# Kernel optimization log

Hardware: AMD Instinct MI355X
Metric: run time of the kernel (lower is better)

The kernel has to match this reference:

```python
import jax, jax.numpy as jnp
import numpy as np


def setup_inputs() -> dict:
    key = jax.random.key(0)
    ks = jax.random.split(key, 8)
    B, C, N = 4, 64, 32768
    d = C // 8
    inp = {
        "x": jax.random.normal(ks[0], (B, C, N), dtype=jnp.float32),
        "Wq": jax.random.normal(ks[1], (d, C), dtype=jnp.float32) * 0.1,
        "bq": jax.random.normal(ks[2], (d,), dtype=jnp.float32) * 0.1,
        "Wk": jax.random.normal(ks[3], (d, C), dtype=jnp.float32) * 0.1,
        "bk": jax.random.normal(ks[4], (d,), dtype=jnp.float32) * 0.1,
        "Wv": jax.random.normal(ks[5], (C, C), dtype=jnp.float32) * 0.1,
        "bv": jax.random.normal(ks[6], (C,), dtype=jnp.float32) * 0.1,
        # nn.Parameter(torch.zeros(1)) in the original; nonzero here so the
        # attention branch actually contributes to the output.
        "gamma": jax.random.normal(ks[7], (1,), dtype=jnp.float32) * 0.1,
        "window_size": 512,
        "stride": 256,
        "pooling_factor": 2,
    }
    return inp


def reference(x, Wq, bq, Wk, bk, Wv, bv, gamma, window_size, stride, pooling_factor):
    B, C, N = x.shape
    # conv1x1 projections are pointwise -> apply once on the full signal
    q = jnp.einsum("dc,bcn->bdn", Wq, x) + bq[None, :, None]  # [B, d, N]
    k = jnp.einsum("dc,bcn->bdn", Wk, x) + bk[None, :, None]  # [B, d, N]
    v = jnp.einsum("ec,bcn->ben", Wv, x) + bv[None, :, None]  # [B, C, N]

    starts = jnp.arange(0, N - window_size + 1, stride)              # [W]
    idx = starts[:, None] + jnp.arange(window_size)[None, :]         # [W, ws]

    qw = q[:, :, idx]  # [B, d, W, ws]
    kw = k[:, :, idx]
    vw = v[:, :, idx]  # [B, C, W, ws]
    xw = x[:, :, idx]

    energy = jnp.einsum("bdwi,bdwj->bwij", qw, kw)                   # [B, W, ws, ws]
    attn = jax.nn.softmax(energy, axis=-1)
    # torch: bmm(v, attn^T) -> out[c,i] = sum_j v[c,j] * attn[i,j]
    out_local = jnp.einsum("bcwj,bwij->bcwi", vw, attn)              # [B, C, W, ws]

    contrib = gamma[0] * out_local + xw
    out = jnp.zeros_like(x).at[:, :, idx].add(contrib)               # overlap-add
    counts = jnp.zeros((N,), x.dtype).at[idx].add(1.0)               # overlap count
    out = out / counts[None, None, :]

    P = pooling_factor
    Np = (N // P) * P
    out = out[:, :, :Np].reshape(B, C, N // P, P).max(axis=-1)       # MaxPool1d(P)
    return out
```

## Files before the change

### kernel.cpp

```cpp
#include <hip/hip_runtime.h>
#include <hip/hip_bf16.h>

#define BB 4
#define CC 64
#define DD 8
#define NN 32768
#define WW 512
#define STR 256
#define NWIN 127
#define LOG2E 1.4426950408889634f

typedef short bf16x8 __attribute__((ext_vector_type(8)));
typedef float f32x4 __attribute__((ext_vector_type(4)));

__device__ __forceinline__ unsigned int pack_bf16(float lo, float hi) {
    __hip_bfloat162 h = __float22bfloat162_rn(make_float2(lo, hi));
    unsigned int r; __builtin_memcpy(&r, &h, 4);
    return r;
}
__device__ __forceinline__ unsigned short to_bf16(float f) {
    __hip_bfloat16 h = __float2bfloat16(f);
    unsigned short r; __builtin_memcpy(&r, &h, 2);
    return r;
}
__device__ __forceinline__ float bf2f(unsigned short s) {
    union { unsigned int u; float f; } v; v.u = ((unsigned int)s) << 16;
    return v.f;
}
__device__ __forceinline__ float fast_exp2(float x) {
#if __has_builtin(__builtin_amdgcn_exp2f)
    return __builtin_amdgcn_exp2f(x);
#else
    float r; asm("v_exp_f32 %0, %1" : "=v"(r) : "v"(x)); return r;
#endif
}
__device__ __forceinline__ bf16x8 pack8(float a0, float a1, float a2, float a3,
                                        float a4, float a5, float a6, float a7) {
    union { bf16x8 v; unsigned int u[4]; } r;
    r.u[0] = pack_bf16(a0, a1); r.u[1] = pack_bf16(a2, a3);
    r.u[2] = pack_bf16(a4, a5); r.u[3] = pack_bf16(a6, a7);
    return r.v;
}

__global__ __launch_bounds__(256) void qkv_kernel(
    const float* __restrict__ x,
    const float* __restrict__ Wq, const float* __restrict__ bq,
    const float* __restrict__ Wk, const float* __restrict__ bk,
    const float* __restrict__ Wv, const float* __restrict__ bv,
    unsigned short* __restrict__ qout, unsigned short* __restrict__ kout,
    unsigned short* __restrict__ vout)
{
    const int t = threadIdx.x;
    const int lane = t & 63, wv = t >> 6;
    const int a = lane & 15, g = lane >> 4;

    bf16x8 wf[5][2];
    #pragma unroll
    for (int T = 0; T < 5; ++T) {
        const float* wrow;
        float scale = 1.f;
        if (T == 0) {
            if (a < 8) { wrow = Wq + a*CC; scale = LOG2E; }
            else       { wrow = Wk + (a-8)*CC; }
        } else {
            wrow = Wv + ((T-1)*16 + a)*CC;
        }
        #pragma unroll
        for (int h = 0; h < 2; ++h) {
            float4 w0 = *(const float4*)(wrow + h*32 + g*8);
            float4 w1 = *(const float4*)(wrow + h*32 + g*8 + 4);
            wf[T][h] = pack8(w0.x*scale, w0.y*scale, w0.z*scale, w0.w*scale,
                             w1.x*scale, w1.y*scale, w1.z*scale, w1.w*scale);
        }
    }
    f32x4 bias[5];
    {
        const int r = g*4;
        #pragma unroll
        for (int u = 0; u < 4; ++u) {
            int rr = r + u;
            bias[0][u] = (rr < 8) ? bq[rr]*LOG2E : bk[rr-8];
        }
        #pragma unroll
        for (int T = 1; T < 5; ++T)
            #pragma unroll
            for (int u = 0; u < 4; ++u)
                bias[T][u] = bv[(T-1)*16 + r + u];
    }

    const int wave_id = blockIdx.x*4 + wv;
    #pragma unroll 1
    for (int it = 0; it < 2; ++it) {
        const int chunk = wave_id + it*4096;
        const int b = chunk >> 11;
        const int n0 = (chunk & 2047) * 16;
        const int n = n0 + a;
        const float* xcol = x + (size_t)b*CC*NN + n;

        float xv0[8], xv1[8];
        #pragma unroll
        for (int u = 0; u < 8; ++u) xv0[u] = xcol[(size_t)(g*8 + u)*NN];
        #pragma unroll
        for (int u = 0; u < 8; ++u) xv1[u] = xcol[(size_t)(32 + g*8 + u)*NN];
        bf16x8 xb0 = pack8(xv0[0],xv0[1],xv0[2],xv0[3],xv0[4],xv0[5],xv0[6],xv0[7]);
        bf16x8 xb1 = pack8(xv1[0],xv1[1],xv1[2],xv1[3],xv1[4],xv1[5],xv1[6],xv1[7]);

        f32x4 acc[5];
        #pragma unroll
        for (int T = 0; T < 5; ++T) {
            acc[T] = __builtin_amdgcn_mfma_f32_16x16x32_bf16(wf[T][0], xb0, bias[T], 0, 0, 0);
            acc[T] = __builtin_amdgcn_mfma_f32_16x16x32_bf16(wf[T][1], xb1, acc[T], 0, 0, 0);
        }

        {
            unsigned int lo = pack_bf16(acc[0][0], acc[0][1]);
            unsigned int hi = pack_bf16(acc[0][2], acc[0][3]);
            unsigned short* base = ((g < 2) ? qout : kout) + ((size_t)b*NN + n)*8 + (g & 1)*4;
            *(int2*)base = make_int2((int)lo, (int)hi);
        }
        #pragma unroll
        for (int T = 1; T < 5; ++T) {
            #pragma unroll
            for (int u = 0; u < 4; ++u) {
                const int e = (T-1)*16 + g*4 + u;
                vout[((size_t)b*CC + e)*NN + n] = to_bf16(acc[T][u]);
            }
        }
    }
}

__global__ __launch_bounds__(256) void attn_kernel(
    const unsigned short* __restrict__ qg, const unsigned short* __restrict__ kg,
    const unsigned short* __restrict__ vg,
    unsigned short* __restrict__ accE, unsigned short* __restrict__ accO)
{
    __shared__ unsigned short sP[4][64][40];
    const int t = threadIdx.x;
    const int lane = t & 63, wv = t >> 6;
    const int a = lane & 15, g = lane >> 4;
    int bid = blockIdx.x;
    const int ih = bid & 1; bid >>= 1;
    const int w = bid % NWIN, b = bid / NWIN;
    const int nwin = STR * w;
    const int i0 = ih*256 + wv*64;

    const unsigned short* qbase = qg + ((size_t)b*NN + nwin + i0)*8;
    const unsigned short* kbase = kg + ((size_t)b*NN + nwin)*8;
    const unsigned short* vbase = vg + (size_t)b*CC*NN + nwin;
    unsigned short* myP = &sP[wv][0][0];

    bf16x8 qf[4];
    #pragma unroll
    for (int nt = 0; nt < 4; ++nt) {
        bf16x8 z = {};
        bf16x8 raw = *(const bf16x8*)(qbase + (size_t)(nt*16 + a)*8);
        qf[nt] = (g == 0) ? raw : z;
    }

    f32x4 acc[4][4] = {};
    float rsum[4] = {0.f, 0.f, 0.f, 0.f};

    bf16x8 kc0 = *(const bf16x8*)(kbase + (size_t)(a)*8);
    bf16x8 kc1 = *(const bf16x8*)(kbase + (size_t)(16 + a)*8);

    for (int jt = 0; jt < 16; ++jt) {
        const int j0 = jt*32;
        bf16x8 vf[4];
        #pragma unroll
        for (int mtc = 0; mtc < 4; ++mtc)
            vf[mtc] = *(const bf16x8*)(vbase + (size_t)(mtc*16 + a)*NN + j0 + g*8);
        bf16x8 kn0, kn1;
        if (jt < 15) {
            kn0 = *(const bf16x8*)(kbase + (size_t)(j0 + 32 + a)*8);
            kn1 = *(const bf16x8*)(kbase + (size_t)(j0 + 48 + a)*8);
        }
        #pragma unroll
        for (int mt = 0; mt < 2; ++mt) {
            const bf16x8 kf = mt ? kc1 : kc0;
            #pragma unroll
            for (int nt = 0; nt < 4; ++nt) {
                f32x4 z4 = {};
                f32x4 e = __builtin_amdgcn_mfma_f32_16x16x32_bf16(kf, qf[nt], z4, 0, 0, 0);
                float p0 = fast_exp2(e[0]), p1 = fast_exp2(e[1]);
                float p2 = fast_exp2(e[2]), p3 = fast_exp2(e[3]);
                rsum[nt] += (p0 + p1) + (p2 + p3);
                int2 pw;
                pw.x = (int)pack_bf16(p0, p1);
                pw.y = (int)pack_bf16(p2, p3);
                *(int2*)(myP + (size_t)(nt*16 + a)*40 + mt*16 + g*4) = pw;
            }
        }
        bf16x8 pf[4];
        #pragma unroll
        for (int nt = 0; nt < 4; ++nt)
            pf[nt] = *(const bf16x8*)(myP + (size_t)(nt*16 + a)*40 + g*8);
        #pragma unroll
        for (int mtc = 0; mtc < 4; ++mtc) {
            #pragma unroll
            for (int nt = 0; nt < 4; ++nt)
                acc[mtc][nt] = __builtin_amdgcn_mfma_f32_16x16x32_bf16(vf[mtc], pf[nt], acc[mtc][nt], 0, 0, 0);
        }
        kc0 = kn0; kc1 = kn1;
    }

    unsigned short* ob = ((w & 1) ? accO : accE) + (size_t)b*CC*NN + nwin + i0;
    #pragma unroll
    for (int nt = 0; nt < 4; ++nt) {
        float r = rsum[nt];
        r += __shfl_xor(r, 16);
        r += __shfl_xor(r, 32);
        const float inv = 1.f / r;
        #pragma unroll
        for (int mtc = 0; mtc < 4; ++mtc) {
            #pragma unroll
            for (int u = 0; u < 4; ++u)
                ob[(size_t)(mtc*16 + g*4 + u)*NN + nt*16 + a] = to_bf16(acc[mtc][nt][u] * inv);
        }
    }
}

__global__ __launch_bounds__(256) void final_kernel(
    const float* __restrict__ x,
    const unsigned short* __restrict__ accE, const unsigned short* __restrict__ accO,
    const float* __restrict__ gamma, float* __restrict__ out)
{
    const size_t tid = (size_t)blockIdx.x*256 + threadIdx.x;
    const size_t base = tid*8;
    const int n = (int)(base & (NN-1));
    const float g = gamma[0];

    float xv[8];
    *(float4*)&xv[0] = *(const float4*)&x[base];
    *(float4*)&xv[4] = *(const float4*)&x[base+4];
    int4 aeq = *(const int4*)&accE[base];
    const unsigned int* ae = (const unsigned int*)&aeq;

    float s[8];
    if (n >= STR && n < NN - STR) {
        int4 aoq = *(const int4*)&accO[base];
        const unsigned int* ao = (const unsigned int*)&aoq;
        #pragma unroll
        for (int u = 0; u < 4; ++u) {
            float e0 = bf2f((unsigned short)(ae[u] & 0xffff));
            float e1 = bf2f((unsigned short)(ae[u] >> 16));
            float o0 = bf2f((unsigned short)(ao[u] & 0xffff));
            float o1 = bf2f((unsigned short)(ao[u] >> 16));
            s[2*u]   = fmaf(g, (e0 + o0)*0.5f, xv[2*u]);
            s[2*u+1] = fmaf(g, (e1 + o1)*0.5f, xv[2*u+1]);
        }
    } else {
        #pragma unroll
        for (int u = 0; u < 4; ++u) {
            float e0 = bf2f((unsigned short)(ae[u] & 0xffff));
            float e1 = bf2f((unsigned short)(ae[u] >> 16));
            s[2*u]   = fmaf(g, e0, xv[2*u]);
            s[2*u+1] = fmaf(g, e1, xv[2*u+1]);
        }
    }
    float4 o = make_float4(fmaxf(s[0], s[1]), fmaxf(s[2], s[3]),
                           fmaxf(s[4], s[5]), fmaxf(s[6], s[7]));
    *(float4*)&out[tid*4] = o;
}

extern "C" void kernel_launch(void* const* d_in, const int* in_sizes, int n_in,
                              void* d_out, int out_size, void* d_ws, size_t ws_size,
                              hipStream_t stream)
{
    const float* x    = (const float*)d_in[0];
    const float* Wq   = (const float*)d_in[1];
    const float* bq   = (const float*)d_in[2];
    const float* Wk   = (const float*)d_in[3];
    const float* bk   = (const float*)d_in[4];
    const float* Wv   = (const float*)d_in[5];
    const float* bv   = (const float*)d_in[6];
    const float* gamma= (const float*)d_in[7];

    unsigned short* q    = (unsigned short*)d_ws;
    unsigned short* k    = q + (size_t)BB*NN*DD;
    unsigned short* v    = k + (size_t)BB*NN*DD;
    unsigned short* accE = v + (size_t)BB*CC*NN;
    unsigned short* accO = accE + (size_t)BB*CC*NN;
    float* out = (float*)d_out;

    qkv_kernel<<<1024, 256, 0, stream>>>(x, Wq, bq, Wk, bk, Wv, bv, q, k, v);
    attn_kernel<<<BB*NWIN*2, 256, 0, stream>>>(q, k, v, accE, accO);
    final_kernel<<<BB*CC*NN/8/256, 256, 0, stream>>>(x, accE, accO, gamma, out);
}
```

Baseline: 82.24 us.

## Switch attention to 32x32x16 MFMA with permlane register reshuffle instead of LDS

```diff
diff --git a/kernel.cpp b/kernel.cpp
--- a/kernel.cpp
+++ b/kernel.cpp
@@ -12,6 +12,7 @@
 
 typedef short bf16x8 __attribute__((ext_vector_type(8)));
 typedef float f32x4 __attribute__((ext_vector_type(4)));
+typedef float f32x16 __attribute__((ext_vector_type(16)));
 
 __device__ __forceinline__ unsigned int pack_bf16(float lo, float hi) {
     __hip_bfloat162 h = __float22bfloat162_rn(make_float2(lo, hi));
@@ -34,11 +35,20 @@
     float r; asm("v_exp_f32 %0, %1" : "=v"(r) : "v"(x)); return r;
 #endif
 }
+__device__ __forceinline__ void plswap(unsigned int &x, unsigned int &y) {
+    asm("v_permlane32_swap_b32 %0, %1" : "+v"(x), "+v"(y));
+}
 __device__ __forceinline__ bf16x8 pack8(float a0, float a1, float a2, float a3,
                                         float a4, float a5, float a6, float a7) {
     union { bf16x8 v; unsigned int u[4]; } r;
     r.u[0] = pack_bf16(a0, a1); r.u[1] = pack_bf16(a2, a3);
     r.u[2] = pack_bf16(a4, a5); r.u[3] = pack_bf16(a6, a7);
+    return r.v;
+}
+__device__ __forceinline__ bf16x8 words4(unsigned int w0, unsigned int w1,
+                                         unsigned int w2, unsigned int w3) {
+    union { bf16x8 v; unsigned int u[4]; } r;
+    r.u[0] = w0; r.u[1] = w1; r.u[2] = w2; r.u[3] = w3;
     return r.v;
 }
 
@@ -134,10 +144,10 @@
     const unsigned short* __restrict__ vg,
     unsigned short* __restrict__ accE, unsigned short* __restrict__ accO)
 {
-    __shared__ unsigned short sP[4][64][40];
+    __shared__ float sInv[4][2][32];
     const int t = threadIdx.x;
     const int lane = t & 63, wv = t >> 6;
-    const int a = lane & 15, g = lane >> 4;
+    const int l31 = lane & 31, hi = lane >> 5;
     int bid = blockIdx.x;
     const int ih = bid & 1; bid >>= 1;
     const int w = bid % NWIN, b = bid / NWIN;
@@ -147,74 +157,95 @@
     const unsigned short* qbase = qg + ((size_t)b*NN + nwin + i0)*8;
     const unsigned short* kbase = kg + ((size_t)b*NN + nwin)*8;
     const unsigned short* vbase = vg + (size_t)b*CC*NN + nwin;
-    unsigned short* myP = &sP[wv][0][0];
-
-    bf16x8 qf[4];
-    #pragma unroll
-    for (int nt = 0; nt < 4; ++nt) {
-        bf16x8 z = {};
-        bf16x8 raw = *(const bf16x8*)(qbase + (size_t)(nt*16 + a)*8);
-        qf[nt] = (g == 0) ? raw : z;
-    }
-
-    f32x4 acc[4][4] = {};
-    float rsum[4] = {0.f, 0.f, 0.f, 0.f};
-
-    bf16x8 kc0 = *(const bf16x8*)(kbase + (size_t)(a)*8);
-    bf16x8 kc1 = *(const bf16x8*)(kbase + (size_t)(16 + a)*8);
+
+    const bf16x8 zf = {};
+    bf16x8 qf[2];
+    #pragma unroll
+    for (int it = 0; it < 2; ++it) {
+        bf16x8 raw = *(const bf16x8*)(qbase + (size_t)(it*32 + l31)*8);
+        qf[it] = hi ? zf : raw;
+    }
+    bf16x8 kc;
+    {
+        bf16x8 raw = *(const bf16x8*)(kbase + (size_t)l31*8);
+        kc = hi ? zf : raw;
+    }
+
+    f32x16 acc[2][2] = {};
+    float rsum[2] = {0.f, 0.f};
 
     for (int jt = 0; jt < 16; ++jt) {
         const int j0 = jt*32;
-        bf16x8 vf[4];
-        #pragma unroll
-        for (int mtc = 0; mtc < 4; ++mtc)
-            vf[mtc] = *(const bf16x8*)(vbase + (size_t)(mtc*16 + a)*NN + j0 + g*8);
-        bf16x8 kn0, kn1;
+        bf16x8 vf[2][2];
+        #pragma unroll
+        for (int ct = 0; ct < 2; ++ct)
+            #pragma unroll
+            for (int sl = 0; sl < 2; ++sl)
+                vf[ct][sl] = *(const bf16x8*)(vbase + (size_t)(ct*32 + l31)*NN + j0 + sl*16 + hi*8);
+        bf16x8 kn = kc;
         if (jt < 15) {
-            kn0 = *(const bf16x8*)(kbase + (size_t)(j0 + 32 + a)*8);
-            kn1 = *(const bf16x8*)(kbase + (size_t)(j0 + 48 + a)*8);
-        }
-        #pragma unroll
-        for (int mt = 0; mt < 2; ++mt) {
-            const bf16x8 kf = mt ? kc1 : kc0;
-            #pragma unroll
-            for (int nt = 0; nt < 4; ++nt) {
-                f32x4 z4 = {};
-                f32x4 e = __builtin_amdgcn_mfma_f32_16x16x32_bf16(kf, qf[nt], z4, 0, 0, 0);
-                float p0 = fast_exp2(e[0]), p1 = fast_exp2(e[1]);
-                float p2 = fast_exp2(e[2]), p3 = fast_exp2(e[3]);
-                rsum[nt] += (p0 + p1) + (p2 + p3);
-                int2 pw;
-                pw.x = (int)pack_bf16(p0, p1);
-                pw.y = (int)pack_bf16(p2, p3);
-                *(int2*)(myP + (size_t)(nt*16 + a)*40 + mt*16 + g*4) = pw;
+            bf16x8 raw = *(const bf16x8*)(kbase + (size_t)(j0 + 32 + l31)*8);
+            kn = hi ? zf : raw;
+        }
+
+        #pragma unroll
+        for (int it = 0; it < 2; ++it) {
+            const f32x16 z16 = {};
+            f32x16 E = __builtin_amdgcn_mfma_f32_32x32x16_bf16(kc, qf[it], z16, 0, 0, 0);
+            float p[16];
+            #pragma unroll
+            for (int r = 0; r < 16; ++r) p[r] = fast_exp2(E[r]);
+            float s01 = (p[0]+p[1]) + (p[2]+p[3]);
+            float s23 = (p[4]+p[5]) + (p[6]+p[7]);
+            float s45 = (p[8]+p[9]) + (p[10]+p[11]);
+            float s67 = (p[12]+p[13]) + (p[14]+p[15]);
+            rsum[it] += (s01+s23) + (s45+s67);
+            unsigned int wd[8];
+            #pragma unroll
+            for (int tw = 0; tw < 8; ++tw) wd[tw] = pack_bf16(p[2*tw], p[2*tw+1]);
+            unsigned int F0 = wd[0], F2 = wd[2]; plswap(F0, F2);
+            unsigned int F1 = wd[1], F3 = wd[3]; plswap(F1, F3);
+            unsigned int G0 = wd[4], G2 = wd[6]; plswap(G0, G2);
+            unsigned int G1 = wd[5], G3 = wd[7]; plswap(G1, G3);
+            bf16x8 pa0 = words4(F0, F1, F2, F3);
+            bf16x8 pa1 = words4(G0, G1, G2, G3);
+            #pragma unroll
+            for (int ct = 0; ct < 2; ++ct) {
+                acc[it][ct] = __builtin_amdgcn_mfma_f32_32x32x16_bf16(pa0, vf[ct][0], acc[it][ct], 0, 0, 0);
+                acc[it][ct] = __builtin_amdgcn_mfma_f32_32x32x16_bf16(pa1, vf[ct][1], acc[it][ct], 0, 0, 0);
             }
         }
-        bf16x8 pf[4];
-        #pragma unroll
-        for (int nt = 0; nt < 4; ++nt)
-            pf[nt] = *(const bf16x8*)(myP + (size_t)(nt*16 + a)*40 + g*8);
-        #pragma unroll
-        for (int mtc = 0; mtc < 4; ++mtc) {
-            #pragma unroll
-            for (int nt = 0; nt < 4; ++nt)
-                acc[mtc][nt] = __builtin_amdgcn_mfma_f32_16x16x32_bf16(vf[mtc], pf[nt], acc[mtc][nt], 0, 0, 0);
-        }
-        kc0 = kn0; kc1 = kn1;
-    }
+        kc = kn;
+    }
+
+    #pragma unroll
+    for (int it = 0; it < 2; ++it) rsum[it] += __shfl_xor(rsum[it], 32);
+    if (lane < 32) {
+        sInv[wv][0][lane] = 1.f / rsum[0];
+        sInv[wv][1][lane] = 1.f / rsum[1];
+    }
+    f32x4 invv[2][4];
+    #pragma unroll
+    for (int it = 0; it < 2; ++it)
+        #pragma unroll
+        for (int g = 0; g < 4; ++g)
+            invv[it][g] = *(const f32x4*)&sInv[wv][it][8*g + 4*hi];
 
     unsigned short* ob = ((w & 1) ? accO : accE) + (size_t)b*CC*NN + nwin + i0;
     #pragma unroll
-    for (int nt = 0; nt < 4; ++nt) {
-        float r = rsum[nt];
-        r += __shfl_xor(r, 16);
-        r += __shfl_xor(r, 32);
-        const float inv = 1.f / r;
-        #pragma unroll
-        for (int mtc = 0; mtc < 4; ++mtc) {
-            #pragma unroll
-            for (int u = 0; u < 4; ++u)
-                ob[(size_t)(mtc*16 + g*4 + u)*NN + nt*16 + a] = to_bf16(acc[mtc][nt][u] * inv);
+    for (int it = 0; it < 2; ++it) {
+        #pragma unroll
+        for (int ct = 0; ct < 2; ++ct) {
+            unsigned short* cbase = ob + (size_t)(ct*32 + l31)*NN + it*32;
+            #pragma unroll
+            for (int g = 0; g < 4; ++g) {
+                float a0 = acc[it][ct][4*g+0] * invv[it][g][0];
+                float a1 = acc[it][ct][4*g+1] * invv[it][g][1];
+                float a2 = acc[it][ct][4*g+2] * invv[it][g][2];
+                float a3 = acc[it][ct][4*g+3] * invv[it][g][3];
+                int2 pw = make_int2((int)pack_bf16(a0, a1), (int)pack_bf16(a2, a3));
+                *(int2*)(cbase + 8*g + 4*hi) = pw;
+            }
         }
     }
 }
```

After: 79.53 us. 1.03x faster.
